# Kernel optimization log

Hardware: AMD Instinct MI355X
Metric: run time of the kernel (lower is better)

Reference implementation:

```python
import jax, jax.numpy as jnp
import numpy as np

B, N, G = 256, 512, 117  # batch, max_num_cells, n_genes
CH = 25                  # Emphsis conv out channels (hidden_d_1st_conv)


def setup_inputs() -> dict:
    key = jax.random.key(0)
    ks = jax.random.split(key, 11)
    images = jax.random.normal(ks[0], (B, N, 1, 7, 7), dtype=jnp.float32)
    spot_images = jax.random.normal(ks[1], (B, 1, 28, 28), dtype=jnp.float32)
    gene_expression = jax.random.normal(ks[2], (B, G), dtype=jnp.float32)
    # Emphsis: Conv2d(1, 25, k=3, s=1) + ReLU
    W_emph = jax.random.normal(ks[3], (CH, 1, 3, 3), dtype=jnp.float32) * 0.2
    b_emph = jax.random.normal(ks[4], (CH,), dtype=jnp.float32) * 0.1
    # 117 stacked GeneBlock Linear(625, 1) heads -> one (G, 625) matrix
    W_reg = jax.random.normal(ks[5], (G, 625), dtype=jnp.float32) * 0.04
    b_reg = jax.random.normal(ks[6], (G,), dtype=jnp.float32) * 0.1
    # PatchEmbedding: Conv2d(1, 3, k=5, s=5)
    W_patch = jax.random.normal(ks[7], (3, 1, 5, 5), dtype=jnp.float32) * 0.2
    b_patch = jax.random.normal(ks[8], (3,), dtype=jnp.float32) * 0.1
    # global_embedding: Linear(75, 1) + ELU
    W_glob = jax.random.normal(ks[9], (1, 75), dtype=jnp.float32) * 0.1
    b_glob = jax.random.normal(ks[10], (1,), dtype=jnp.float32) * 0.1
    return dict(images=images, spot_images=spot_images, gene_expression=gene_expression,
                W_emph=W_emph, b_emph=b_emph, W_reg=W_reg, b_reg=b_reg,
                W_patch=W_patch, b_patch=b_patch, W_glob=W_glob, b_glob=b_glob)


def reference(images, spot_images, gene_expression, W_emph, b_emph, W_reg, b_reg,
              W_patch, b_patch, W_glob, b_glob):
    Bn, Nc = images.shape[0], images.shape[1]
    # Emphsis conv over all (batch, cell) pairs at once: (B*N, 1, 7, 7) -> (B*N, 25, 5, 5)
    x = images.reshape(Bn * Nc, 1, 7, 7)
    t = jax.lax.conv_general_dilated(x, W_emph, window_strides=(1, 1), padding='VALID',
                                     dimension_numbers=('NCHW', 'OIHW', 'NCHW'))
    t = jax.nn.relu(t + b_emph[None, :, None, None])
    flat = t.reshape(Bn, Nc, CH * 5 * 5)  # (B, N, 625)
    # 117 independent Linear(625,1) heads fused into one matmul -> (B, N, G)
    out = jnp.einsum('bnd,gd->bng', flat, W_reg) + b_reg
    # PatchEmbedding: (B,1,28,28) -> (B,3,5,5) -> tokens (B,25,3) -> flatten (B,75)
    s = jax.lax.conv_general_dilated(spot_images, W_patch, window_strides=(5, 5), padding='VALID',
                                     dimension_numbers=('NCHW', 'OIHW', 'NCHW'))
    s = s + b_patch[None, :, None, None]
    s = s.reshape(Bn, 3, 25).transpose(0, 2, 1).reshape(Bn, 75)
    glob = jax.nn.elu(s @ W_glob.T + b_glob)  # (B, 1)
    # out1 broadcast of global embedding over (cells, genes)
    cell = jax.nn.relu(out + glob[:, :, None])  # (B, N, G)
    # F.linear with ones weight over cell axis == sum over cells
    spot = cell.sum(axis=1)  # (B, G)
    out1 = jnp.broadcast_to(glob[:, :, None], (Bn, Nc, out.shape[2]))  # (B, N, G)
    return spot, cell, out1
```

## Files before the change

### kernel.cpp

```cpp
#include <hip/hip_runtime.h>


typedef __attribute__((ext_vector_type(16))) float f32x16;
typedef __attribute__((ext_vector_type(8))) short short8;
typedef __attribute__((ext_vector_type(2))) unsigned int uint2v;
typedef __attribute__((ext_vector_type(4))) unsigned int uint4v;

#define WCOMB_OFF 0
#define GLOB_OFF  245760

#define SPOT_OUT_OFF 0
#define CELL_OUT_OFF 29952
#define OUT1_OUT_OFF 15365376

#define SMEM_BYTES 155648

__device__ __forceinline__ unsigned short f2bf(float x) {
  unsigned int u = __builtin_bit_cast(unsigned int, x);
  u = (u + 0x7FFFu + ((u >> 16) & 1u)) >> 16;
  return (unsigned short)u;
}

__device__ __forceinline__ unsigned int cvt_pk_bf16(float lo, float hi) {
  unsigned int w;
  asm("v_cvt_pk_bf16_f32 %0, %1, %2" : "=v"(w) : "v"(lo), "v"(hi));
  return w;
}

__device__ __forceinline__ void gload16(const void* g, void* l) {
  __builtin_amdgcn_global_load_lds(
      (const __attribute__((address_space(1))) void*)g,
      (__attribute__((address_space(3))) void*)l, 16, 0, 0);
}

__global__ __launch_bounds__(128) void prep_kernel(
    const float* __restrict__ spot_images, const float* __restrict__ W_patch,
    const float* __restrict__ b_patch, const float* __restrict__ W_glob,
    const float* __restrict__ b_glob, const float* __restrict__ W_reg,
    const float* __restrict__ W_emph, const float* __restrict__ b_emph,
    unsigned short* __restrict__ wcomb, float* __restrict__ glob) {
  int bid = blockIdx.x;
  int tid = threadIdx.x;
  if (bid < 256) {
    __shared__ float red[75];
    if (tid < 75) {
      int token = tid / 3;
      int chan = tid - token * 3;
      int ty = token / 5, tx = token - ty * 5;
      const float* img = spot_images + bid * 784 + (ty * 5) * 28 + tx * 5;
      float a = 0.f;
      #pragma unroll
      for (int i = 0; i < 5; ++i)
        #pragma unroll
        for (int j = 0; j < 5; ++j)
          a = fmaf(img[i * 28 + j], W_patch[chan * 25 + i * 5 + j], a);
      a += b_patch[chan];
      red[tid] = a * W_glob[tid];
    }
    __syncthreads();
    if (tid == 0) {
      float s = b_glob[0];
      for (int k = 0; k < 75; ++k) s += red[k];
      glob[bid] = (s > 0.f) ? s : expm1f(s);
    }
  } else if (bid < 336) {
    int idx = bid - 256;
    int jt = idx >> 2, s = idx & 3;
    if (tid < 64) {
      int j = jt * 32 + (tid & 31);
      int h = tid >> 5;
      unsigned short hv[8];
      #pragma unroll
      for (int jj = 0; jj < 8; ++jj) {
        int i = s * 16 + h * 8 + jj;
        float val = 0.f;
        if (j < 625) {
          int ch = j / 25, p = j % 25;
          int oy = p / 5, ox = p - oy * 5;
          if (i < 49) {
            int iy = i / 7, ix = i - iy * 7;
            int ky = iy - oy, kx = ix - ox;
            if (ky >= 0 && ky < 3 && kx >= 0 && kx < 3)
              val = W_emph[ch * 9 + ky * 3 + kx];
          } else if (i == 49) {
            val = b_emph[ch];
          }
        }
        hv[jj] = f2bf(val);
      }
      unsigned int u[4];
      #pragma unroll
      for (int k = 0; k < 4; ++k)
        u[k] = (unsigned int)hv[2 * k] | ((unsigned int)hv[2 * k + 1] << 16);
      ((uint4*)wcomb)[jt * 768 + s * 64 + tid] = make_uint4(u[0], u[1], u[2], u[3]);
    }
  } else {
    int idx = bid - 336;
    int sg = idx >> 2, q = idx & 3;
    if (tid < 64) {
      int g = q * 32 + (tid & 31);
      int h = tid >> 5;
      unsigned short hv[8];
      #pragma unroll
      for (int jj = 0; jj < 8; ++jj) {
        int k = sg * 16 + h * 8 + jj;
        float val = (g < 117 && k < 625) ? W_reg[g * 625 + k] : 0.f;
        hv[jj] = f2bf(val);
      }
      unsigned int u[4];
      #pragma unroll
      for (int k = 0; k < 4; ++k)
        u[k] = (unsigned int)hv[2 * k] | ((unsigned int)hv[2 * k + 1] << 16);
      int jt = sg >> 1, c = (sg & 1) * 4 + q;
      ((uint4*)wcomb)[jt * 768 + 256 + c * 64 + tid] =
          make_uint4(u[0], u[1], u[2], u[3]);
    }
  }
}

__global__ __launch_bounds__(512, 2) void main_kernel(
    const float* __restrict__ images, const float* __restrict__ b_reg,
    const unsigned short* __restrict__ wcomb, const float* __restrict__ glob,
    float* __restrict__ out) {
  extern __shared__ char smem[];
  unsigned short* imgbs = (unsigned short*)smem;
  char* wslab = smem + 32768;
  float* redp = (float*)smem;
  int tid = threadIdx.x;
  int b = blockIdx.x;
  int l = tid & 63;
  int ct = __builtin_amdgcn_readfirstlane(tid >> 6);
  int m = l & 31, hh = l >> 5;
  const char* wcombB = (const char*)wcomb;
  const short8* imgb8 = (const short8*)imgbs;

  float gb = glob[b];
  size_t rowbase = (size_t)b * 512;
  float4 gv = make_float4(gb, gb, gb, gb);
  float4* o1v = (float4*)(out + OUT1_OUT_OFF + rowbase * 117);

  auto stage_half = [&](int h) {
    #pragma unroll
    for (int i = 0; i < 15; ++i) {
      int c = ct + 8 * i;
      gload16(wcombB + h * 122880 + c * 1024 + l * 16, wslab + c * 1024);
    }
  };

  auto stageimg = [&](int hf) {
    #pragma unroll
    for (int it = 0; it < 4; ++it) {
      int u = it * 512 + tid;
      int cell = u & 255, kc = u >> 8;
      const float* src =
          images + (size_t)(b * 512 + hf * 256 + cell) * 49 + kc * 8;
      float v[8];
      #pragma unroll
      for (int j = 0; j < 8; ++j) v[j] = 0.f;
      if (kc < 6) {
        #pragma unroll
        for (int j = 0; j < 8; ++j) v[j] = src[j];
      } else if (kc == 6) {
        v[0] = src[0];
        v[1] = 1.0f;
      }
      unsigned int uu[4];
      #pragma unroll
      for (int k = 0; k < 4; ++k) uu[k] = cvt_pk_bf16(v[2 * k], v[2 * k + 1]);
      ((uint4*)imgbs)[kc * 256 + cell] = make_uint4(uu[0], uu[1], uu[2], uu[3]);
    }
  };

  short8 bU0, bU1, bU2, bU3, bV0, bV1, bV2, bV3;
  int base = (ct & 3) * 64;
  stageimg(0);
  __syncthreads();
  if (ct < 4) {
    bU0 = imgb8[(0 + hh) * 256 + base + m];
    bU1 = imgb8[(2 + hh) * 256 + base + m];
    bU2 = imgb8[(4 + hh) * 256 + base + m];
    bU3 = imgb8[(6 + hh) * 256 + base + m];
    bV0 = imgb8[(0 + hh) * 256 + base + 32 + m];
    bV1 = imgb8[(2 + hh) * 256 + base + 32 + m];
    bV2 = imgb8[(4 + hh) * 256 + base + 32 + m];
    bV3 = imgb8[(6 + hh) * 256 + base + 32 + m];
  }
  __syncthreads();
  stageimg(1);
  __syncthreads();
  if (ct >= 4) {
    bU0 = imgb8[(0 + hh) * 256 + base + m];
    bU1 = imgb8[(2 + hh) * 256 + base + m];
    bU2 = imgb8[(4 + hh) * 256 + base + m];
    bU3 = imgb8[(6 + hh) * 256 + base + m];
    bV0 = imgb8[(0 + hh) * 256 + base + 32 + m];
    bV1 = imgb8[(2 + hh) * 256 + base + 32 + m];
    bV2 = imgb8[(4 + hh) * 256 + base + 32 + m];
    bV3 = imgb8[(6 + hh) * 256 + base + 32 + m];
  }
  stage_half(0);
  __syncthreads();

  f32x16 aU0, aU1, aU2, aU3, aV0, aV1, aV2, aV3;
  #pragma unroll
  for (int i = 0; i < 16; ++i) {
    aU0[i] = 0.f; aU1[i] = 0.f; aU2[i] = 0.f; aU3[i] = 0.f;
    aV0[i] = 0.f; aV1[i] = 0.f; aV2[i] = 0.f; aV3[i] = 0.f;
  }

  auto body = [&](int jl, int jt) {
    if (jt < 15) {
      int i0 = jt * 1024 + tid;
      o1v[i0] = gv;
      int i1 = i0 + 512;
      if (i1 < 14976) o1v[i1] = gv;
    }
    const short8* wB = (const short8*)(wslab + jl * 12288);
    short8 a0 = wB[l];
    short8 a1 = wB[64 + l];
    short8 a2 = wB[128 + l];
    short8 a3 = wB[192 + l];

    f32x16 o;
    #pragma unroll
    for (int i = 0; i < 16; ++i) o[i] = 0.f;
    o = __builtin_amdgcn_mfma_f32_32x32x16_bf16(a0, bU0, o, 0, 0, 0);
    o = __builtin_amdgcn_mfma_f32_32x32x16_bf16(a1, bU1, o, 0, 0, 0);
    o = __builtin_amdgcn_mfma_f32_32x32x16_bf16(a2, bU2, o, 0, 0, 0);
    o = __builtin_amdgcn_mfma_f32_32x32x16_bf16(a3, bU3, o, 0, 0, 0);
    unsigned int W[8];
    #pragma unroll
    for (int q = 0; q < 8; ++q)
      W[q] = cvt_pk_bf16(fmaxf(o[2 * q], 0.f), fmaxf(o[2 * q + 1], 0.f));
    uint2v s02 = __builtin_amdgcn_permlane32_swap(W[0], W[2], false, false);
    uint2v s13 = __builtin_amdgcn_permlane32_swap(W[1], W[3], false, false);
    uint2v s46 = __builtin_amdgcn_permlane32_swap(W[4], W[6], false, false);
    uint2v s57 = __builtin_amdgcn_permlane32_swap(W[5], W[7], false, false);
    uint4v f0 = {s02[0], s13[0], s02[1], s13[1]};
    uint4v f1 = {s46[0], s57[0], s46[1], s57[1]};
    short8 afU0 = __builtin_bit_cast(short8, f0);
    short8 afU1 = __builtin_bit_cast(short8, f1);

    #pragma unroll
    for (int i = 0; i < 16; ++i) o[i] = 0.f;
    o = __builtin_amdgcn_mfma_f32_32x32x16_bf16(a0, bV0, o, 0, 0, 0);
    o = __builtin_amdgcn_mfma_f32_32x32x16_bf16(a1, bV1, o, 0, 0, 0);
    o = __builtin_amdgcn_mfma_f32_32x32x16_bf16(a2, bV2, o, 0, 0, 0);
    o = __builtin_amdgcn_mfma_f32_32x32x16_bf16(a3, bV3, o, 0, 0, 0);
    #pragma unroll
    for (int q = 0; q < 8; ++q)
      W[q] = cvt_pk_bf16(fmaxf(o[2 * q], 0.f), fmaxf(o[2 * q + 1], 0.f));
    s02 = __builtin_amdgcn_permlane32_swap(W[0], W[2], false, false);
    s13 = __builtin_amdgcn_permlane32_swap(W[1], W[3], false, false);
    s46 = __builtin_amdgcn_permlane32_swap(W[4], W[6], false, false);
    s57 = __builtin_amdgcn_permlane32_swap(W[5], W[7], false, false);
    uint4v g0 = {s02[0], s13[0], s02[1], s13[1]};
    uint4v g1 = {s46[0], s57[0], s46[1], s57[1]};
    short8 afV0 = __builtin_bit_cast(short8, g0);
    short8 afV1 = __builtin_bit_cast(short8, g1);

    #define MM2(c, AFU, AFV, AU, AV)                                        \
      {                                                                     \
        short8 w = wB[256 + (c)*64 + l];                                    \
        AU = __builtin_amdgcn_mfma_f32_32x32x16_bf16(AFU, w, AU, 0, 0, 0);  \
        AV = __builtin_amdgcn_mfma_f32_32x32x16_bf16(AFV, w, AV, 0, 0, 0);  \
      }
    MM2(0, afU0, afV0, aU0, aV0)
    MM2(1, afU0, afV0, aU1, aV1)
    MM2(2, afU0, afV0, aU2, aV2)
    MM2(3, afU0, afV0, aU3, aV3)
    MM2(4, afU1, afV1, aU0, aV0)
    MM2(5, afU1, afV1, aU1, aV1)
    MM2(6, afU1, afV1, aU2, aV2)
    MM2(7, afU1, afV1, aU3, aV3)
    #undef MM2
  };

  for (int jl = 0; jl < 10; ++jl) body(jl, jl);
  __syncthreads();
  stage_half(1);
  __syncthreads();
  for (int jl = 0; jl < 10; ++jl) body(jl, 10 + jl);

  float br0 = (m < 117) ? b_reg[m] : 0.f;
  float br1 = b_reg[32 + m];
  float br2 = b_reg[64 + m];
  float br3 = (96 + m < 117) ? b_reg[96 + m] : 0.f;

  {
    auto rsum = [&](const f32x16& AU, const f32x16& AV, float br) {
      float s = 0.f;
      #pragma unroll
      for (int reg = 0; reg < 16; ++reg)
        s += fmaxf(AU[reg] + br + gb, 0.f) + fmaxf(AV[reg] + br + gb, 0.f);
      s += __shfl_xor(s, 32, 64);
      return s;
    };
    float s0 = rsum(aU0, aV0, br0);
    float s1 = rsum(aU1, aV1, br1);
    float s2 = rsum(aU2, aV2, br2);
    float s3 = rsum(aU3, aV3, br3);
    if (hh == 0) {
      redp[ct * 128 + m] = s0;
      redp[ct * 128 + 32 + m] = s1;
      redp[ct * 128 + 64 + m] = s2;
      redp[ct * 128 + 96 + m] = s3;
    }
  }
  __syncthreads();
  if (tid < 117) {
    float s = 0.f;
    #pragma unroll
    for (int w = 0; w < 8; ++w) s += redp[w * 128 + tid];
    out[SPOT_OUT_OFF + b * 117 + tid] = s;
  }

  bool q3ok = (m < 21);
  float* cbase = out + CELL_OUT_OFF + (rowbase + ct * 64 + 4 * hh) * 117 + m;
  #pragma unroll
  for (int G = 0; G < 4; ++G) {
    float* pU = cbase + (8 * G) * 117;
    float* pV = pU + 32 * 117;
    #pragma unroll
    for (int rr = 0; rr < 4; ++rr) {
      int r = G * 4 + rr;
      int ro = rr * 117;
      pU[ro] = fmaxf(aU0[r] + br0 + gb, 0.f);
      pU[ro + 32] = fmaxf(aU1[r] + br1 + gb, 0.f);
      pU[ro + 64] = fmaxf(aU2[r] + br2 + gb, 0.f);
      if (q3ok) pU[ro + 96] = fmaxf(aU3[r] + br3 + gb, 0.f);
      pV[ro] = fmaxf(aV0[r] + br0 + gb, 0.f);
      pV[ro + 32] = fmaxf(aV1[r] + br1 + gb, 0.f);
      pV[ro + 64] = fmaxf(aV2[r] + br2 + gb, 0.f);
      if (q3ok) pV[ro + 96] = fmaxf(aV3[r] + br3 + gb, 0.f);
    }
  }
}

extern "C" void kernel_launch(void* const* d_in, const int* in_sizes, int n_in,
                              void* d_out, int out_size, void* d_ws, size_t ws_size,
                              hipStream_t stream) {
  const float* images      = (const float*)d_in[0];
  const float* spot_images = (const float*)d_in[1];
  const float* W_emph = (const float*)d_in[3];
  const float* b_emph = (const float*)d_in[4];
  const float* W_reg  = (const float*)d_in[5];
  const float* b_reg  = (const float*)d_in[6];
  const float* W_patch = (const float*)d_in[7];
  const float* b_patch = (const float*)d_in[8];
  const float* W_glob  = (const float*)d_in[9];
  const float* b_glob  = (const float*)d_in[10];
  float* out = (float*)d_out;

  unsigned short* wcomb = (unsigned short*)((char*)d_ws + WCOMB_OFF);
  float* glob  = (float*)((char*)d_ws + GLOB_OFF);

  (void)hipFuncSetAttribute((const void*)main_kernel,
                            hipFuncAttributeMaxDynamicSharedMemorySize,
                            SMEM_BYTES);

  prep_kernel<<<496, 128, 0, stream>>>(spot_images, W_patch, b_patch, W_glob,
                                       b_glob, W_reg, W_emph, b_emph, wcomb,
                                       glob);
  main_kernel<<<256, 512, SMEM_BYTES, stream>>>(images, b_reg, wcomb, glob,
                                                out);
}
```

Baseline: 51.83 us.

## Fuse prep kernel into main kernel, building bf16 weights in LDS per block

Removes the separate prep kernel launch: each block now computes its own global embedding scalar and builds the combined bf16 conv-im2col and regression weight slab directly in shared memory from fp32 inputs. This eliminates a kernel launch and the workspace round trip. In exchange, every block redundantly recomputes the weight transformation and reads W_reg in fp32 with strided access instead of async-copying a prepacked slab.

```diff
diff --git a/kernel.cpp b/kernel.cpp
--- a/kernel.cpp
+++ b/kernel.cpp
@@ -6,20 +6,11 @@
 typedef __attribute__((ext_vector_type(2))) unsigned int uint2v;
 typedef __attribute__((ext_vector_type(4))) unsigned int uint4v;
 
-#define WCOMB_OFF 0
-#define GLOB_OFF  245760
-
 #define SPOT_OUT_OFF 0
 #define CELL_OUT_OFF 29952
 #define OUT1_OUT_OFF 15365376
 
 #define SMEM_BYTES 155648
-
-__device__ __forceinline__ unsigned short f2bf(float x) {
-  unsigned int u = __builtin_bit_cast(unsigned int, x);
-  u = (u + 0x7FFFu + ((u >> 16) & 1u)) >> 16;
-  return (unsigned short)u;
-}
 
 __device__ __forceinline__ unsigned int cvt_pk_bf16(float lo, float hi) {
   unsigned int w;
@@ -27,123 +18,103 @@
   return w;
 }
 
-__device__ __forceinline__ void gload16(const void* g, void* l) {
-  __builtin_amdgcn_global_load_lds(
-      (const __attribute__((address_space(1))) void*)g,
-      (__attribute__((address_space(3))) void*)l, 16, 0, 0);
-}
-
-__global__ __launch_bounds__(128) void prep_kernel(
-    const float* __restrict__ spot_images, const float* __restrict__ W_patch,
-    const float* __restrict__ b_patch, const float* __restrict__ W_glob,
-    const float* __restrict__ b_glob, const float* __restrict__ W_reg,
+__global__ __launch_bounds__(512, 2) void main_kernel(
+    const float* __restrict__ images, const float* __restrict__ spot_images,
+    const float* __restrict__ W_patch, const float* __restrict__ b_patch,
+    const float* __restrict__ W_glob, const float* __restrict__ b_glob,
     const float* __restrict__ W_emph, const float* __restrict__ b_emph,
-    unsigned short* __restrict__ wcomb, float* __restrict__ glob) {
-  int bid = blockIdx.x;
-  int tid = threadIdx.x;
-  if (bid < 256) {
-    __shared__ float red[75];
-    if (tid < 75) {
-      int token = tid / 3;
-      int chan = tid - token * 3;
-      int ty = token / 5, tx = token - ty * 5;
-      const float* img = spot_images + bid * 784 + (ty * 5) * 28 + tx * 5;
-      float a = 0.f;
-      #pragma unroll
-      for (int i = 0; i < 5; ++i)
-        #pragma unroll
-        for (int j = 0; j < 5; ++j)
-          a = fmaf(img[i * 28 + j], W_patch[chan * 25 + i * 5 + j], a);
-      a += b_patch[chan];
-      red[tid] = a * W_glob[tid];
-    }
-    __syncthreads();
-    if (tid == 0) {
-      float s = b_glob[0];
-      for (int k = 0; k < 75; ++k) s += red[k];
-      glob[bid] = (s > 0.f) ? s : expm1f(s);
-    }
-  } else if (bid < 336) {
-    int idx = bid - 256;
-    int jt = idx >> 2, s = idx & 3;
-    if (tid < 64) {
-      int j = jt * 32 + (tid & 31);
-      int h = tid >> 5;
-      unsigned short hv[8];
-      #pragma unroll
-      for (int jj = 0; jj < 8; ++jj) {
-        int i = s * 16 + h * 8 + jj;
-        float val = 0.f;
-        if (j < 625) {
-          int ch = j / 25, p = j % 25;
-          int oy = p / 5, ox = p - oy * 5;
-          if (i < 49) {
-            int iy = i / 7, ix = i - iy * 7;
-            int ky = iy - oy, kx = ix - ox;
-            if (ky >= 0 && ky < 3 && kx >= 0 && kx < 3)
-              val = W_emph[ch * 9 + ky * 3 + kx];
-          } else if (i == 49) {
-            val = b_emph[ch];
-          }
-        }
-        hv[jj] = f2bf(val);
-      }
-      unsigned int u[4];
-      #pragma unroll
-      for (int k = 0; k < 4; ++k)
-        u[k] = (unsigned int)hv[2 * k] | ((unsigned int)hv[2 * k + 1] << 16);
-      ((uint4*)wcomb)[jt * 768 + s * 64 + tid] = make_uint4(u[0], u[1], u[2], u[3]);
-    }
-  } else {
-    int idx = bid - 336;
-    int sg = idx >> 2, q = idx & 3;
-    if (tid < 64) {
-      int g = q * 32 + (tid & 31);
-      int h = tid >> 5;
-      unsigned short hv[8];
-      #pragma unroll
-      for (int jj = 0; jj < 8; ++jj) {
-        int k = sg * 16 + h * 8 + jj;
-        float val = (g < 117 && k < 625) ? W_reg[g * 625 + k] : 0.f;
-        hv[jj] = f2bf(val);
-      }
-      unsigned int u[4];
-      #pragma unroll
-      for (int k = 0; k < 4; ++k)
-        u[k] = (unsigned int)hv[2 * k] | ((unsigned int)hv[2 * k + 1] << 16);
-      int jt = sg >> 1, c = (sg & 1) * 4 + q;
-      ((uint4*)wcomb)[jt * 768 + 256 + c * 64 + tid] =
-          make_uint4(u[0], u[1], u[2], u[3]);
-    }
-  }
-}
-
-__global__ __launch_bounds__(512, 2) void main_kernel(
-    const float* __restrict__ images, const float* __restrict__ b_reg,
-    const unsigned short* __restrict__ wcomb, const float* __restrict__ glob,
+    const float* __restrict__ W_reg, const float* __restrict__ b_reg,
     float* __restrict__ out) {
   extern __shared__ char smem[];
   unsigned short* imgbs = (unsigned short*)smem;
   char* wslab = smem + 32768;
+  float* gred = (float*)smem;
   float* redp = (float*)smem;
   int tid = threadIdx.x;
   int b = blockIdx.x;
   int l = tid & 63;
   int ct = __builtin_amdgcn_readfirstlane(tid >> 6);
   int m = l & 31, hh = l >> 5;
-  const char* wcombB = (const char*)wcomb;
   const short8* imgb8 = (const short8*)imgbs;
 
-  float gb = glob[b];
+  if (tid < 75) {
+    int token = tid / 3;
+    int chan = tid - token * 3;
+    int ty = token / 5, tx = token - ty * 5;
+    const float* img = spot_images + b * 784 + (ty * 5) * 28 + tx * 5;
+    float a = 0.f;
+    #pragma unroll
+    for (int i = 0; i < 5; ++i)
+      #pragma unroll
+      for (int j = 0; j < 5; ++j)
+        a = fmaf(img[i * 28 + j], W_patch[chan * 25 + i * 5 + j], a);
+    a += b_patch[chan];
+    gred[tid] = a * W_glob[tid];
+  }
+  __syncthreads();
+  if (tid == 0) {
+    float s = b_glob[0];
+    for (int k = 0; k < 75; ++k) s += gred[k];
+    gred[80] = (s > 0.f) ? s : expm1f(s);
+  }
+  __syncthreads();
+  float gb = gred[80];
+  __syncthreads();
+
   size_t rowbase = (size_t)b * 512;
   float4 gv = make_float4(gb, gb, gb, gb);
   float4* o1v = (float4*)(out + OUT1_OUT_OFF + rowbase * 117);
 
-  auto stage_half = [&](int h) {
-    #pragma unroll
-    for (int i = 0; i < 15; ++i) {
-      int c = ct + 8 * i;
-      gload16(wcombB + h * 122880 + c * 1024 + l * 16, wslab + c * 1024);
+  auto convert_half = [&](int h) {
+    #pragma unroll
+    for (int it = 0; it < 15; ++it) {
+      int u = it * 8 + ct;
+      unsigned int u4[4];
+      char* dst;
+      if (u < 40) {
+        int jt_local = u >> 2, s = u & 3;
+        int j = (h * 10 + jt_local) * 32 + m;
+        bool jok = (j < 625);
+        int ch = j / 25, p = j - ch * 25;
+        int oy = p / 5, ox = p - oy * 5;
+        int i0 = s * 16 + hh * 8;
+        float v[8];
+        #pragma unroll
+        for (int jj = 0; jj < 8; ++jj) {
+          int i = i0 + jj;
+          float val = 0.f;
+          if (jok) {
+            if (i < 49) {
+              int iy = i / 7, ix = i - iy * 7;
+              int ky = iy - oy, kx = ix - ox;
+              if (ky >= 0 && ky < 3 && kx >= 0 && kx < 3)
+                val = W_emph[ch * 9 + ky * 3 + kx];
+            } else if (i == 49) {
+              val = b_emph[ch];
+            }
+          }
+          v[jj] = val;
+        }
+        #pragma unroll
+        for (int k = 0; k < 4; ++k) u4[k] = cvt_pk_bf16(v[2 * k], v[2 * k + 1]);
+        dst = wslab + jt_local * 12288 + s * 1024 + l * 16;
+      } else {
+        int widx = u - 40;
+        int sg_local = widx >> 2, q = widx & 3;
+        int g = q * 32 + m;
+        bool gok = (g < 117);
+        int k0 = (h * 20 + sg_local) * 16 + hh * 8;
+        const float* wr = W_reg + g * 625 + k0;
+        float v[8];
+        #pragma unroll
+        for (int jj = 0; jj < 8; ++jj)
+          v[jj] = (gok && (k0 + jj) < 625) ? wr[jj] : 0.f;
+        #pragma unroll
+        for (int k = 0; k < 4; ++k) u4[k] = cvt_pk_bf16(v[2 * k], v[2 * k + 1]);
+        dst = wslab + (sg_local >> 1) * 12288 + 4096 +
+              ((sg_local & 1) * 4 + q) * 1024 + l * 16;
+      }
+      *(uint4*)dst = make_uint4(u4[0], u4[1], u4[2], u4[3]);
     }
   };
 
@@ -198,7 +169,7 @@
     bV2 = imgb8[(4 + hh) * 256 + base + 32 + m];
     bV3 = imgb8[(6 + hh) * 256 + base + 32 + m];
   }
-  stage_half(0);
+  convert_half(0);
   __syncthreads();
 
   f32x16 aU0, aU1, aU2, aU3, aV0, aV1, aV2, aV3;
@@ -278,11 +249,11 @@
 
   for (int jl = 0; jl < 10; ++jl) body(jl, jl);
   __syncthreads();
-  stage_half(1);
+  convert_half(1);
   __syncthreads();
   for (int jl = 0; jl < 10; ++jl) body(jl, 10 + jl);
 
-  float br0 = (m < 117) ? b_reg[m] : 0.f;
+  float br0 = b_reg[m];
   float br1 = b_reg[32 + m];
   float br2 = b_reg[64 + m];
   float br3 = (96 + m < 117) ? b_reg[96 + m] : 0.f;
@@ -352,16 +323,11 @@
   const float* b_glob  = (const float*)d_in[10];
   float* out = (float*)d_out;
 
-  unsigned short* wcomb = (unsigned short*)((char*)d_ws + WCOMB_OFF);
-  float* glob  = (float*)((char*)d_ws + GLOB_OFF);
-
   (void)hipFuncSetAttribute((const void*)main_kernel,
                             hipFuncAttributeMaxDynamicSharedMemorySize,
                             SMEM_BYTES);
 
-  prep_kernel<<<496, 128, 0, stream>>>(spot_images, W_patch, b_patch, W_glob,
-                                       b_glob, W_reg, W_emph, b_emph, wcomb,
-                                       glob);
-  main_kernel<<<256, 512, SMEM_BYTES, stream>>>(images, b_reg, wcomb, glob,
-                                                out);
+  main_kernel<<<256, 512, SMEM_BYTES, stream>>>(
+      images, spot_images, W_patch, b_patch, W_glob, b_glob, W_emph, b_emph,
+      W_reg, b_reg, out);
 }
```

Result: slower. 76.25 us (+47.1%).

## Read combined weights directly from global memory instead of staging through LDS

Applied to the files above, without the earlier changes.

Removes the global_load_lds staging of the combined weight slab into a 120KB LDS buffer and reads the weights per iteration straight from global memory (via L2/L1 cache). LDS usage drops to static image and reduction buffers, and the two-half loop with its barriers becomes one 20-iteration loop. This cuts LDS footprint and synchronisation, but weight fetches now have global-memory latency inside the MFMA loop with no explicit prefetch.

```diff
diff --git a/kernel.cpp b/kernel.cpp
--- a/kernel.cpp
+++ b/kernel.cpp
@@ -13,8 +13,6 @@
 #define CELL_OUT_OFF 29952
 #define OUT1_OUT_OFF 15365376
 
-#define SMEM_BYTES 155648
-
 __device__ __forceinline__ unsigned short f2bf(float x) {
   unsigned int u = __builtin_bit_cast(unsigned int, x);
   u = (u + 0x7FFFu + ((u >> 16) & 1u)) >> 16;
@@ -25,12 +23,6 @@
   unsigned int w;
   asm("v_cvt_pk_bf16_f32 %0, %1, %2" : "=v"(w) : "v"(lo), "v"(hi));
   return w;
-}
-
-__device__ __forceinline__ void gload16(const void* g, void* l) {
-  __builtin_amdgcn_global_load_lds(
-      (const __attribute__((address_space(1))) void*)g,
-      (__attribute__((address_space(3))) void*)l, 16, 0, 0);
 }
 
 __global__ __launch_bounds__(128) void prep_kernel(
@@ -122,30 +114,20 @@
     const float* __restrict__ images, const float* __restrict__ b_reg,
     const unsigned short* __restrict__ wcomb, const float* __restrict__ glob,
     float* __restrict__ out) {
-  extern __shared__ char smem[];
-  unsigned short* imgbs = (unsigned short*)smem;
-  char* wslab = smem + 32768;
-  float* redp = (float*)smem;
+  __shared__ unsigned short imgbs[8 * 256 * 8];
+  __shared__ float redp[8 * 128];
   int tid = threadIdx.x;
   int b = blockIdx.x;
   int l = tid & 63;
   int ct = __builtin_amdgcn_readfirstlane(tid >> 6);
   int m = l & 31, hh = l >> 5;
-  const char* wcombB = (const char*)wcomb;
   const short8* imgb8 = (const short8*)imgbs;
+  const short8* wc8 = (const short8*)wcomb;
 
   float gb = glob[b];
   size_t rowbase = (size_t)b * 512;
   float4 gv = make_float4(gb, gb, gb, gb);
   float4* o1v = (float4*)(out + OUT1_OUT_OFF + rowbase * 117);
-
-  auto stage_half = [&](int h) {
-    #pragma unroll
-    for (int i = 0; i < 15; ++i) {
-      int c = ct + 8 * i;
-      gload16(wcombB + h * 122880 + c * 1024 + l * 16, wslab + c * 1024);
-    }
-  };
 
   auto stageimg = [&](int hf) {
     #pragma unroll
@@ -198,8 +180,6 @@
     bV2 = imgb8[(4 + hh) * 256 + base + 32 + m];
     bV3 = imgb8[(6 + hh) * 256 + base + 32 + m];
   }
-  stage_half(0);
-  __syncthreads();
 
   f32x16 aU0, aU1, aU2, aU3, aV0, aV1, aV2, aV3;
   #pragma unroll
@@ -208,14 +188,14 @@
     aV0[i] = 0.f; aV1[i] = 0.f; aV2[i] = 0.f; aV3[i] = 0.f;
   }
 
-  auto body = [&](int jl, int jt) {
+  for (int jt = 0; jt < 20; ++jt) {
     if (jt < 15) {
       int i0 = jt * 1024 + tid;
       o1v[i0] = gv;
       int i1 = i0 + 512;
       if (i1 < 14976) o1v[i1] = gv;
     }
-    const short8* wB = (const short8*)(wslab + jl * 12288);
+    const short8* wB = wc8 + jt * 768;
     short8 a0 = wB[l];
     short8 a1 = wB[64 + l];
     short8 a2 = wB[128 + l];
@@ -274,15 +254,9 @@
     MM2(6, afU1, afV1, aU2, aV2)
     MM2(7, afU1, afV1, aU3, aV3)
     #undef MM2
-  };
-
-  for (int jl = 0; jl < 10; ++jl) body(jl, jl);
-  __syncthreads();
-  stage_half(1);
-  __syncthreads();
-  for (int jl = 0; jl < 10; ++jl) body(jl, 10 + jl);
-
-  float br0 = (m < 117) ? b_reg[m] : 0.f;
+  }
+
+  float br0 = b_reg[m];
   float br1 = b_reg[32 + m];
   float br2 = b_reg[64 + m];
   float br3 = (96 + m < 117) ? b_reg[96 + m] : 0.f;
@@ -355,13 +329,8 @@
   unsigned short* wcomb = (unsigned short*)((char*)d_ws + WCOMB_OFF);
   float* glob  = (float*)((char*)d_ws + GLOB_OFF);
 
-  (void)hipFuncSetAttribute((const void*)main_kernel,
-                            hipFuncAttributeMaxDynamicSharedMemorySize,
-                            SMEM_BYTES);
-
   prep_kernel<<<496, 128, 0, stream>>>(spot_images, W_patch, b_patch, W_glob,
                                        b_glob, W_reg, W_emph, b_emph, wcomb,
                                        glob);
-  main_kernel<<<256, 512, SMEM_BYTES, stream>>>(images, b_reg, wcomb, glob,
-                                                out);
-}
+  main_kernel<<<256, 512, 0, stream>>>(images, b_reg, wcomb, glob, out);
+}
```

After: 54.69 us. 5.5% more time.
